# Optimization experiments

Measured on AMD Instinct MI355X. Metric: run time of the kernel, lower is better.

## Reference

```python
import jax, jax.numpy as jnp
import numpy as np

TEMPERATURE = 0.5
EPS = 1e-8  # torch CosineSimilarity eps


def setup_inputs() -> dict:
    key = jax.random.key(0)
    # x holds 2*batch_size concatenated embeddings (two augmented views)
    x = jax.random.normal(key, (4096, 512), dtype=jnp.float32)
    return {"x": x}


def reference(x) -> jnp.ndarray:
    n2 = x.shape[0]          # 2N rows
    n = n2 // 2
    # cosine similarity: normalize rows (clamped norm as in torch), then GEMM
    norms = jnp.maximum(jnp.linalg.norm(x, axis=1, keepdims=True), EPS)
    xn = x / norms
    sim = jnp.einsum('id,jd->ij', xn, xn) / TEMPERATURE  # [2N, 2N]
    # positive logit for row i is sim[i, (i+N) mod 2N]
    idx = jnp.arange(n2)
    pos = sim[idx, (idx + n) % n2]
    # CE with label 0 over logits = [pos, negatives]; since the logit set for
    # row i is exactly {sim[i, j] : j != i}, CE_i = logsumexp_{j!=i} sim[i,j] - pos_i
    sim_masked = jnp.where(jnp.eye(n2, dtype=bool), -jnp.inf, sim)
    lse = jax.nn.logsumexp(sim_masked, axis=1)
    # criterion uses reduction='sum' then divides by bsz -> mean
    return jnp.mean(lse - pos)
```

## Files before the change

kernel.cpp:

```cpp
#include <hip/hip_runtime.h>
#include <hip/hip_bf16.h>
#include <math.h>

typedef __bf16 bf16_t;
typedef __bf16 bf16x8 __attribute__((ext_vector_type(8)));
typedef float f32x4 __attribute__((ext_vector_type(4)));

#define N2 4096
#define NHALF 2048
#define DIM 512
#define TEMP_INV 2.0f

__global__ __launch_bounds__(256) void k_prep(const float* __restrict__ x,
                                              bf16_t* __restrict__ xn,
                                              float* __restrict__ pos,
                                              float* __restrict__ diag,
                                              float* __restrict__ rowsum) {
    const int pair = blockIdx.x * 4 + (threadIdx.x >> 6);
    const int lane = threadIdx.x & 63;
    const int rowi = pair;
    const int rowp = pair + NHALF;

    const float4* xi = reinterpret_cast<const float4*>(x + (size_t)rowi * DIM);
    const float4* xp = reinterpret_cast<const float4*>(x + (size_t)rowp * DIM);
    float4 a0 = xi[lane * 2], a1 = xi[lane * 2 + 1];
    float4 b0 = xp[lane * 2], b1 = xp[lane * 2 + 1];

    float ssi = a0.x*a0.x + a0.y*a0.y + a0.z*a0.z + a0.w*a0.w
              + a1.x*a1.x + a1.y*a1.y + a1.z*a1.z + a1.w*a1.w;
    float ssp = b0.x*b0.x + b0.y*b0.y + b0.z*b0.z + b0.w*b0.w
              + b1.x*b1.x + b1.y*b1.y + b1.z*b1.z + b1.w*b1.w;
    float dot = a0.x*b0.x + a0.y*b0.y + a0.z*b0.z + a0.w*b0.w
              + a1.x*b1.x + a1.y*b1.y + a1.z*b1.z + a1.w*b1.w;
#pragma unroll
    for (int off = 32; off; off >>= 1) {
        ssi += __shfl_xor(ssi, off, 64);
        ssp += __shfl_xor(ssp, off, 64);
        dot += __shfl_xor(dot, off, 64);
    }
    const float ni = fmaxf(sqrtf(ssi), 1e-8f);
    const float np = fmaxf(sqrtf(ssp), 1e-8f);
    const float sci = 1.0f / ni, scp = 1.0f / np;

    float va[8] = {a0.x, a0.y, a0.z, a0.w, a1.x, a1.y, a1.z, a1.w};
    float vb[8] = {b0.x, b0.y, b0.z, b0.w, b1.x, b1.y, b1.z, b1.w};
    bf16x8 oi, op;
    float dii = 0.0f, dpp = 0.0f;
#pragma unroll
    for (int t = 0; t < 8; ++t) {
        oi[t] = (bf16_t)(va[t] * sci);
        op[t] = (bf16_t)(vb[t] * scp);
        float fi = (float)oi[t], fp_ = (float)op[t];
        dii += fi * fi;
        dpp += fp_ * fp_;
    }
    *reinterpret_cast<bf16x8*>(xn + (size_t)rowi * DIM + lane * 8) = oi;
    *reinterpret_cast<bf16x8*>(xn + (size_t)rowp * DIM + lane * 8) = op;
#pragma unroll
    for (int off = 32; off; off >>= 1) {
        dii += __shfl_xor(dii, off, 64);
        dpp += __shfl_xor(dpp, off, 64);
    }
    if (lane == 0) {
        const float pv = TEMP_INV * dot * sci * scp;
        pos[rowi] = pv;
        pos[rowp] = pv;
        diag[rowi] = TEMP_INV * dii;
        diag[rowp] = TEMP_INV * dpp;
    }
    if (threadIdx.x < 8) rowsum[blockIdx.x * 8 + threadIdx.x] = 0.0f;
}

__device__ __forceinline__ void load_lds16(const bf16_t* g, bf16_t* l) {
    __builtin_amdgcn_global_load_lds(
        (const __attribute__((address_space(1))) unsigned int*)g,
        (__attribute__((address_space(3))) unsigned int*)l,
        16, 0, 0);
}

__global__ __launch_bounds__(256) void k_simgemm(const bf16_t* __restrict__ xn,
                                                 float* __restrict__ rowsum) {
    __shared__ bf16_t As[2][128 * 32];
    __shared__ bf16_t Bs[2][128 * 32];
    __shared__ float  rpA[128];
    __shared__ float  rpB[128];

    const int t = blockIdx.x;
    int bn = (int)((sqrtf(8.0f * (float)t + 1.0f) - 1.0f) * 0.5f);
    while ((bn * (bn + 1)) / 2 > t) --bn;
    while (((bn + 1) * (bn + 2)) / 2 <= t) ++bn;
    const int bm = t - (bn * (bn + 1)) / 2;
    const bool diagb = (bm == bn);

    const int tid  = threadIdx.x;
    const int lane = tid & 63;
    const int wid  = tid >> 6;
    const int wr   = wid >> 1;
    const int wc   = wid & 1;
    const int q    = lane >> 4;
    const int l15  = lane & 15;

    if (tid < 128) { rpA[tid] = 0.0f; rpB[tid] = 0.0f; }

    const bf16_t* gA = xn + (size_t)(bm * 128 + (tid >> 2)) * DIM + (tid & 3) * 8;
    const bf16_t* gB = xn + (size_t)(bn * 128 + (tid >> 2)) * DIM + (tid & 3) * 8;

    f32x4 acc[4][4] = {};

    load_lds16(gA,                    &As[0][tid * 8]);
    load_lds16(gA + (size_t)64 * DIM, &As[0][2048 + tid * 8]);
    load_lds16(gB,                    &Bs[0][tid * 8]);
    load_lds16(gB + (size_t)64 * DIM, &Bs[0][2048 + tid * 8]);

#pragma unroll
    for (int kt = 0; kt < 16; ++kt) {
        const int cur = kt & 1;
        if (kt < 15) {
            const bf16_t* gA1 = gA + (size_t)(kt + 1) * 32;
            const bf16_t* gB1 = gB + (size_t)(kt + 1) * 32;
            load_lds16(gA1,                    &As[cur ^ 1][tid * 8]);
            load_lds16(gA1 + (size_t)64 * DIM, &As[cur ^ 1][2048 + tid * 8]);
            load_lds16(gB1,                    &Bs[cur ^ 1][tid * 8]);
            load_lds16(gB1 + (size_t)64 * DIM, &Bs[cur ^ 1][2048 + tid * 8]);
            asm volatile("s_waitcnt vmcnt(4)" ::: "memory");
        } else {
            asm volatile("s_waitcnt vmcnt(0)" ::: "memory");
        }
        __builtin_amdgcn_s_barrier();

        bf16x8 af[4], bv[4];
#pragma unroll
        for (int mt = 0; mt < 4; ++mt)
            af[mt] = *reinterpret_cast<const bf16x8*>(
                &As[cur][(wr * 64 + mt * 16 + l15) * 32 + q * 8]);
#pragma unroll
        for (int nt = 0; nt < 4; ++nt)
            bv[nt] = *reinterpret_cast<const bf16x8*>(
                &Bs[cur][(wc * 64 + nt * 16 + l15) * 32 + q * 8]);
#pragma unroll
        for (int mt = 0; mt < 4; ++mt)
#pragma unroll
            for (int nt = 0; nt < 4; ++nt)
                acc[mt][nt] = __builtin_amdgcn_mfma_f32_16x16x32_bf16(
                    af[mt], bv[nt], acc[mt][nt], 0, 0, 0);
        __builtin_amdgcn_s_barrier();
    }

    float colacc[4] = {0.0f, 0.0f, 0.0f, 0.0f};
#pragma unroll
    for (int mt = 0; mt < 4; ++mt) {
        float rowp[4] = {0.0f, 0.0f, 0.0f, 0.0f};
#pragma unroll
        for (int nt = 0; nt < 4; ++nt)
#pragma unroll
            for (int r = 0; r < 4; ++r) {
                float e = __expf(TEMP_INV * acc[mt][nt][r]);
                rowp[r] += e;
                colacc[nt] += e;
            }
#pragma unroll
        for (int r = 0; r < 4; ++r) {
            float p = rowp[r];
            p += __shfl_xor(p, 1, 64);
            p += __shfl_xor(p, 2, 64);
            p += __shfl_xor(p, 4, 64);
            p += __shfl_xor(p, 8, 64);
            if (l15 == 0) atomicAdd(&rpA[wr * 64 + mt * 16 + q * 4 + r], p);
        }
    }
    if (!diagb) {
#pragma unroll
        for (int nt = 0; nt < 4; ++nt) {
            float c = colacc[nt];
            c += __shfl_xor(c, 16, 64);
            c += __shfl_xor(c, 32, 64);
            if (q == 0) atomicAdd(&rpB[wc * 64 + nt * 16 + l15], c);
        }
    }
    __syncthreads();
    if (tid < 128) {
        atomicAdd(&rowsum[bm * 128 + tid], rpA[tid]);
    } else if (!diagb) {
        atomicAdd(&rowsum[bn * 128 + (tid - 128)], rpB[tid - 128]);
    }
}

__global__ __launch_bounds__(256) void k_finalize(const float* __restrict__ rowsum,
                                                  const float* __restrict__ pos,
                                                  const float* __restrict__ diag,
                                                  float* __restrict__ out) {
    __shared__ float red[256];
    const float4* rs4 = reinterpret_cast<const float4*>(rowsum);
    const float4* ps4 = reinterpret_cast<const float4*>(pos);
    const float4* dg4 = reinterpret_cast<const float4*>(diag);
    float s = 0.0f;
#pragma unroll
    for (int it = 0; it < 4; ++it) {
        const int i = it * 256 + threadIdx.x;
        float4 r = rs4[i];
        float4 p = ps4[i];
        float4 d = dg4[i];
        s += __logf(r.x - __expf(d.x)) - p.x;
        s += __logf(r.y - __expf(d.y)) - p.y;
        s += __logf(r.z - __expf(d.z)) - p.z;
        s += __logf(r.w - __expf(d.w)) - p.w;
    }
    red[threadIdx.x] = s;
    __syncthreads();
    for (int st = 128; st; st >>= 1) {
        if (threadIdx.x < st) red[threadIdx.x] += red[threadIdx.x + st];
        __syncthreads();
    }
    if (threadIdx.x == 0) out[0] = red[0] / (float)N2;
}

extern "C" void kernel_launch(void* const* d_in, const int* in_sizes, int n_in,
                              void* d_out, int out_size, void* d_ws, size_t ws_size,
                              hipStream_t stream) {
    (void)in_sizes; (void)n_in; (void)out_size; (void)ws_size;
    const float* x = (const float*)d_in[0];
    float* out = (float*)d_out;

    char* ws = (char*)d_ws;
    bf16_t* xn     = (bf16_t*)ws;
    float*  rowsum = (float*)(ws + (size_t)N2 * DIM * 2);
    float*  pos    = rowsum + N2;
    float*  diag   = pos + N2;

    k_prep<<<512, 256, 0, stream>>>(x, xn, pos, diag, rowsum);
    k_simgemm<<<528, 256, 0, stream>>>(xn, rowsum);
    k_finalize<<<1, 256, 0, stream>>>(rowsum, pos, diag, out);
}
```

Baseline: 84.25 us.

## Triple-buffer GEMM LDS tiles with one barrier per step and XOR swizzle

The similarity GEMM now uses a three-stage LDS ring with prefetch distance two instead of double buffering. This lets each k-step drop the trailing barrier, leaving a single barrier per iteration. Global-to-LDS chunk placement and the fragment read addresses are XOR-swizzled to reduce LDS bank conflicts on the 16-byte fragment loads. The cost is more shared memory per block, which may lower occupancy, and more complex wait-count reasoning.

```diff
diff --git a/kernel.cpp b/kernel.cpp
--- a/kernel.cpp
+++ b/kernel.cpp
@@ -80,8 +80,8 @@
 
 __global__ __launch_bounds__(256) void k_simgemm(const bf16_t* __restrict__ xn,
                                                  float* __restrict__ rowsum) {
-    __shared__ bf16_t As[2][128 * 32];
-    __shared__ bf16_t Bs[2][128 * 32];
+    __shared__ bf16_t As[3][128 * 32];
+    __shared__ bf16_t Bs[3][128 * 32];
     __shared__ float  rpA[128];
     __shared__ float  rpB[128];
 
@@ -102,48 +102,56 @@
 
     if (tid < 128) { rpA[tid] = 0.0f; rpB[tid] = 0.0f; }
 
-    const bf16_t* gA = xn + (size_t)(bm * 128 + (tid >> 2)) * DIM + (tid & 3) * 8;
-    const bf16_t* gB = xn + (size_t)(bn * 128 + (tid >> 2)) * DIM + (tid & 3) * 8;
+    const int slot_g = (tid & 3) ^ ((tid >> 3) & 3);
+    const bf16_t* gA = xn + (size_t)(bm * 128 + (tid >> 2)) * DIM + slot_g * 8;
+    const bf16_t* gB = xn + (size_t)(bn * 128 + (tid >> 2)) * DIM + slot_g * 8;
+
+    const int rsw = (q ^ ((l15 >> 1) & 3)) * 8;
+    const int arow = (wr * 64 + l15) * 32 + rsw;
+    const int brow = (wc * 64 + l15) * 32 + rsw;
 
     f32x4 acc[4][4] = {};
 
-    load_lds16(gA,                    &As[0][tid * 8]);
-    load_lds16(gA + (size_t)64 * DIM, &As[0][2048 + tid * 8]);
-    load_lds16(gB,                    &Bs[0][tid * 8]);
-    load_lds16(gB + (size_t)64 * DIM, &Bs[0][2048 + tid * 8]);
+    load_lds16(gA,                         &As[0][tid * 8]);
+    load_lds16(gA + (size_t)64 * DIM,      &As[0][2048 + tid * 8]);
+    load_lds16(gB,                         &Bs[0][tid * 8]);
+    load_lds16(gB + (size_t)64 * DIM,      &Bs[0][2048 + tid * 8]);
+    load_lds16(gA + 32,                    &As[1][tid * 8]);
+    load_lds16(gA + (size_t)64 * DIM + 32, &As[1][2048 + tid * 8]);
+    load_lds16(gB + 32,                    &Bs[1][tid * 8]);
+    load_lds16(gB + (size_t)64 * DIM + 32, &Bs[1][2048 + tid * 8]);
 
 #pragma unroll
     for (int kt = 0; kt < 16; ++kt) {
-        const int cur = kt & 1;
-        if (kt < 15) {
-            const bf16_t* gA1 = gA + (size_t)(kt + 1) * 32;
-            const bf16_t* gB1 = gB + (size_t)(kt + 1) * 32;
-            load_lds16(gA1,                    &As[cur ^ 1][tid * 8]);
-            load_lds16(gA1 + (size_t)64 * DIM, &As[cur ^ 1][2048 + tid * 8]);
-            load_lds16(gB1,                    &Bs[cur ^ 1][tid * 8]);
-            load_lds16(gB1 + (size_t)64 * DIM, &Bs[cur ^ 1][2048 + tid * 8]);
-            asm volatile("s_waitcnt vmcnt(4)" ::: "memory");
-        } else {
-            asm volatile("s_waitcnt vmcnt(0)" ::: "memory");
+        if (kt < 15) asm volatile("s_waitcnt vmcnt(4)" ::: "memory");
+        else         asm volatile("s_waitcnt vmcnt(0)" ::: "memory");
+        __builtin_amdgcn_s_barrier();
+        __builtin_amdgcn_sched_barrier(0);
+
+        if (kt + 2 < 16) {
+            const int nb = (kt + 2) % 3;
+            const bf16_t* gA2 = gA + (kt + 2) * 32;
+            const bf16_t* gB2 = gB + (kt + 2) * 32;
+            load_lds16(gA2,                    &As[nb][tid * 8]);
+            load_lds16(gA2 + (size_t)64 * DIM, &As[nb][2048 + tid * 8]);
+            load_lds16(gB2,                    &Bs[nb][tid * 8]);
+            load_lds16(gB2 + (size_t)64 * DIM, &Bs[nb][2048 + tid * 8]);
         }
-        __builtin_amdgcn_s_barrier();
-
+
+        const int cb = kt % 3;
         bf16x8 af[4], bv[4];
 #pragma unroll
         for (int mt = 0; mt < 4; ++mt)
-            af[mt] = *reinterpret_cast<const bf16x8*>(
-                &As[cur][(wr * 64 + mt * 16 + l15) * 32 + q * 8]);
+            af[mt] = *reinterpret_cast<const bf16x8*>(&As[cb][arow + mt * 512]);
 #pragma unroll
         for (int nt = 0; nt < 4; ++nt)
-            bv[nt] = *reinterpret_cast<const bf16x8*>(
-                &Bs[cur][(wc * 64 + nt * 16 + l15) * 32 + q * 8]);
+            bv[nt] = *reinterpret_cast<const bf16x8*>(&Bs[cb][brow + nt * 512]);
 #pragma unroll
         for (int mt = 0; mt < 4; ++mt)
 #pragma unroll
             for (int nt = 0; nt < 4; ++nt)
                 acc[mt][nt] = __builtin_amdgcn_mfma_f32_16x16x32_bf16(
                     af[mt], bv[nt], acc[mt][nt], 0, 0, 0);
-        __builtin_amdgcn_s_barrier();
     }
 
     float colacc[4] = {0.0f, 0.0f, 0.0f, 0.0f};
```

Result: faster. 78.77 us, median of 2 (-6.5%).

## Load GEMM operand fragments directly from global memory, dropping LDS staging

Applied to the files above, without the earlier changes.

The similarity GEMM no longer stages A/B tiles through double-buffered shared memory with global_load_lds. Each wave now reads its MFMA operand fragments straight from global memory (via L1/L2) inside the fully unrolled K loop, which removes the per-iteration barriers and waitcnts. The cost is that each operand row is fetched redundantly by the two waves that share it, and the loads are less coalesced. Performance now depends on cache hit rates and on how well the compiler schedules the unrolled loads.

```diff
diff --git a/kernel.cpp b/kernel.cpp
--- a/kernel.cpp
+++ b/kernel.cpp
@@ -71,19 +71,10 @@
     if (threadIdx.x < 8) rowsum[blockIdx.x * 8 + threadIdx.x] = 0.0f;
 }
 
-__device__ __forceinline__ void load_lds16(const bf16_t* g, bf16_t* l) {
-    __builtin_amdgcn_global_load_lds(
-        (const __attribute__((address_space(1))) unsigned int*)g,
-        (__attribute__((address_space(3))) unsigned int*)l,
-        16, 0, 0);
-}
-
 __global__ __launch_bounds__(256) void k_simgemm(const bf16_t* __restrict__ xn,
                                                  float* __restrict__ rowsum) {
-    __shared__ bf16_t As[2][128 * 32];
-    __shared__ bf16_t Bs[2][128 * 32];
-    __shared__ float  rpA[128];
-    __shared__ float  rpB[128];
+    __shared__ float rpA[128];
+    __shared__ float rpB[128];
 
     const int t = blockIdx.x;
     int bn = (int)((sqrtf(8.0f * (float)t + 1.0f) - 1.0f) * 0.5f);
@@ -102,49 +93,35 @@
 
     if (tid < 128) { rpA[tid] = 0.0f; rpB[tid] = 0.0f; }
 
-    const bf16_t* gA = xn + (size_t)(bm * 128 + (tid >> 2)) * DIM + (tid & 3) * 8;
-    const bf16_t* gB = xn + (size_t)(bn * 128 + (tid >> 2)) * DIM + (tid & 3) * 8;
+    const bf16_t* aP[4];
+    const bf16_t* bP[4];
+#pragma unroll
+    for (int mt = 0; mt < 4; ++mt)
+        aP[mt] = xn + (size_t)(bm * 128 + wr * 64 + mt * 16 + l15) * DIM + q * 8;
+#pragma unroll
+    for (int nt = 0; nt < 4; ++nt)
+        bP[nt] = xn + (size_t)(bn * 128 + wc * 64 + nt * 16 + l15) * DIM + q * 8;
 
     f32x4 acc[4][4] = {};
 
-    load_lds16(gA,                    &As[0][tid * 8]);
-    load_lds16(gA + (size_t)64 * DIM, &As[0][2048 + tid * 8]);
-    load_lds16(gB,                    &Bs[0][tid * 8]);
-    load_lds16(gB + (size_t)64 * DIM, &Bs[0][2048 + tid * 8]);
-
 #pragma unroll
     for (int kt = 0; kt < 16; ++kt) {
-        const int cur = kt & 1;
-        if (kt < 15) {
-            const bf16_t* gA1 = gA + (size_t)(kt + 1) * 32;
-            const bf16_t* gB1 = gB + (size_t)(kt + 1) * 32;
-            load_lds16(gA1,                    &As[cur ^ 1][tid * 8]);
-            load_lds16(gA1 + (size_t)64 * DIM, &As[cur ^ 1][2048 + tid * 8]);
-            load_lds16(gB1,                    &Bs[cur ^ 1][tid * 8]);
-            load_lds16(gB1 + (size_t)64 * DIM, &Bs[cur ^ 1][2048 + tid * 8]);
-            asm volatile("s_waitcnt vmcnt(4)" ::: "memory");
-        } else {
-            asm volatile("s_waitcnt vmcnt(0)" ::: "memory");
-        }
-        __builtin_amdgcn_s_barrier();
-
         bf16x8 af[4], bv[4];
 #pragma unroll
         for (int mt = 0; mt < 4; ++mt)
-            af[mt] = *reinterpret_cast<const bf16x8*>(
-                &As[cur][(wr * 64 + mt * 16 + l15) * 32 + q * 8]);
+            af[mt] = *reinterpret_cast<const bf16x8*>(aP[mt] + kt * 32);
 #pragma unroll
         for (int nt = 0; nt < 4; ++nt)
-            bv[nt] = *reinterpret_cast<const bf16x8*>(
-                &Bs[cur][(wc * 64 + nt * 16 + l15) * 32 + q * 8]);
+            bv[nt] = *reinterpret_cast<const bf16x8*>(bP[nt] + kt * 32);
 #pragma unroll
         for (int mt = 0; mt < 4; ++mt)
 #pragma unroll
             for (int nt = 0; nt < 4; ++nt)
                 acc[mt][nt] = __builtin_amdgcn_mfma_f32_16x16x32_bf16(
                     af[mt], bv[nt], acc[mt][nt], 0, 0, 0);
-        __builtin_amdgcn_s_barrier();
-    }
+    }
+
+    __syncthreads();
 
     float colacc[4] = {0.0f, 0.0f, 0.0f, 0.0f};
 #pragma unroll
```

After: 110.3 us. +30.9%, slower.
